# Kernel optimization log

Hardware: AMD Instinct MI355X
Metric: run time of the kernel (lower is better)

The kernel has to match this reference:

```python
import jax, jax.numpy as jnp
import numpy as np

B, C, N, V, H = 8, 256, 1024, 12, 4
D = C // H  # 64
BN_EPS = 1e-5
NEG = 1e10


def _vconv(x, W, b, g, bt, m4):
    """VointConv block: 1x1 conv + BN(batch stats) + relu, with reset_voint_mask
    applied after every sublayer (as in the torch loop).
    x: [B, Cin, N, V], W: [Cout, Cin], m4: [B, 1, N, V] float mask."""
    y = (jnp.einsum('oc,bcnv->bonv', W, x) + b[None, :, None, None]) * m4
    mu = jnp.mean(y, axis=(0, 2, 3), keepdims=True)
    var = jnp.var(y, axis=(0, 2, 3), keepdims=True)
    y = ((y - mu) * jax.lax.rsqrt(var + BN_EPS) * g[None, :, None, None]
         + bt[None, :, None, None]) * m4
    return jax.nn.relu(y) * m4


def setup_inputs() -> dict:
    key = jax.random.key(0)
    ks = jax.random.split(key, 20)
    inp = {}
    inp['voints_feats'] = jax.random.normal(ks[0], (B, C, N, V), jnp.float32)
    inp['voints_mask'] = (jax.random.uniform(ks[1], (B, N, V)) > 0.3).astype(jnp.float32)
    w = lambda k, shp: (jax.random.normal(k, shp, jnp.float32) * 0.05)
    # embed_layers[0]: VointConv([C, C/heads])
    inp['We'] = w(ks[2], (D, C)); inp['be'] = w(ks[3], (D,))
    inp['ge'] = 1.0 + 0.1 * jax.random.normal(ks[4], (D,), jnp.float32)
    inp['bne'] = 0.1 * jax.random.normal(ks[5], (D,), jnp.float32)
    # embed_atten_layers[0]: VointConv([C/heads, 3*C])
    inp['Wa'] = w(ks[6], (3 * C, D)); inp['ba'] = w(ks[7], (3 * C,))
    inp['ga'] = 1.0 + 0.1 * jax.random.normal(ks[8], (3 * C,), jnp.float32)
    inp['bna'] = 0.1 * jax.random.normal(ks[9], (3 * C,), jnp.float32)
    # to_out[0]: VointConv([C, C])
    inp['Wo'] = w(ks[10], (C, C)); inp['bo'] = w(ks[11], (C,))
    inp['go'] = 1.0 + 0.1 * jax.random.normal(ks[12], (C,), jnp.float32)
    inp['bno'] = 0.1 * jax.random.normal(ks[13], (C,), jnp.float32)
    # feedforward[0]: VointConv([C, C])
    inp['Wf'] = w(ks[14], (C, C)); inp['bf'] = w(ks[15], (C,))
    inp['gf'] = 1.0 + 0.1 * jax.random.normal(ks[16], (C,), jnp.float32)
    inp['bnf'] = 0.1 * jax.random.normal(ks[17], (C,), jnp.float32)
    return inp


def reference(voints_feats, voints_mask, We, be, ge, bne, Wa, ba, ga, bna,
              Wo, bo, go, bno, Wf, bf, gf, bnf):
    mask = voints_mask                      # [B, N, V] float
    m4 = mask[:, None, :, :]                # [B, 1, N, V]
    # embedding to per-head dim, then joint QKV projection
    emb = _vconv(voints_feats, We, be, ge, bne, m4)      # [B, D, N, V]
    qkv = _vconv(emb, Wa, ba, ga, bna, m4)               # [B, 3C, N, V]
    k, q, v = jnp.split(qkv, 3, axis=1)                  # torch.chunk order: k, q, v
    resh = lambda t: t.reshape(B, H, D, N, V)            # 'b (h d) n v -> b h d n v'
    q, k, v = resh(q), resh(k), resh(v)
    scale = float(C) ** (-0.5)
    dots = jnp.einsum('bhdnv,bhdnj->bhnvj', q, k) * scale  # [B,H,N,V,V]
    empty = jnp.sum(mask, axis=-1) == 0                  # [B, N]
    dots = jnp.where(empty[:, None, :, None, None], 0.0, dots)
    # vointsoftmax: bias broadcasts over query dim v (mask[...,None] -> [B,1,N,V,1])
    qbias = jnp.where(mask[:, None, :, :, None] > 0, 0.0, -NEG)
    attn = jax.nn.softmax(dots + qbias, axis=-1) * mask[:, None, :, :, None]
    # faithful to source: 'b h n v j, b h d n v -> b h n v d' (j summed over attn only)
    out = jnp.einsum('bhnvj,bhdnv->bhnvd', attn, v)      # [B,H,N,V,D]
    out = out.transpose(0, 1, 4, 2, 3).reshape(B, C, N, V)  # 'b h n v d -> b (h d) n v'
    out = jnp.where(empty[:, None, :, None], 0.0, out)
    out = _vconv(out, Wo, bo, go, bno, m4)
    x = voints_feats + out
    x = x + _vconv(x, Wf, bf, gf, bnf, m4)
    return x
```

## Files before the change

kernel.cpp:

```cpp
#include <hip/hip_runtime.h>
#include <hip/hip_bf16.h>

typedef __attribute__((ext_vector_type(8))) __bf16 bf16x8;
typedef __attribute__((ext_vector_type(4))) float floatx4;
typedef __attribute__((ext_vector_type(8))) unsigned short ushort8;

namespace {
constexpr int kC  = 256;
constexpr int kNV = 1024 * 12;
constexpr int kP  = 8 * kNV;
constexpr float kEps = 1e-5f;

constexpr size_t OFF_PART   = 2048;
constexpr size_t OFF_WB     = 2048 + 16384;
constexpr size_t OFF_XT     = OFF_WB + 81920;
constexpr size_t OFF_Y1     = OFF_XT + (size_t)kP * 256 / 2;
constexpr size_t OFF_Y2     = OFF_Y1 + (size_t)kP * 64 / 2;
constexpr size_t OFF_Y3     = OFF_Y2 + (size_t)kP * 256 / 2;
}

__device__ __forceinline__ unsigned short f2bf(float f) {
    unsigned int u = __builtin_bit_cast(unsigned int, f);
    u += 0x7FFFu + ((u >> 16) & 1u);
    return (unsigned short)(u >> 16);
}
__device__ __forceinline__ float bf2f(unsigned short h) {
    unsigned int u = ((unsigned int)h) << 16;
    return __builtin_bit_cast(float, u);
}

__global__ void convw_kernel(const float* __restrict__ We, const float* __restrict__ Wa,
                             const float* __restrict__ Wo, const float* __restrict__ Wf,
                             unsigned short* __restrict__ dst)
{
    const int f = (blockIdx.x * 256 + threadIdx.x) * 4;
    const float* src; int off, M, K, base;
    if (f < 16384)      { src = We;            off = f;         M = 64;  K = 256; base = 0; }
    else if (f < 32768) { src = Wa + 512 * 64; off = f - 16384; M = 256; K = 64;  base = 16384; }
    else if (f < 98304) { src = Wo;            off = f - 32768; M = 256; K = 256; base = 32768; }
    else                { src = Wf;            off = f - 98304; M = 256; K = 256; base = 98304; }
    const int m = off / K, k = off - m * K;
    const float4 v = *(const float4*)&src[off];
    ushort4 o; o.x = f2bf(v.x); o.y = f2bf(v.y); o.z = f2bf(v.z); o.w = f2bf(v.w);
    *(ushort4*)&dst[base + (k >> 5) * (M * 32) + m * 32 + (k & 31)] = o;
}

__global__ __launch_bounds__(256) void transpose_kernel(
    const float* __restrict__ x, unsigned short* __restrict__ xT)
{
    __shared__ float T[64][65];
    const int p0 = blockIdx.x * 64;
    const int c0 = blockIdx.y * 64;
    const int b  = p0 / kNV;
    const int q0 = p0 - b * kNV;
    const int t  = threadIdx.x;

    const int cl = t >> 2;
    const int pq = (t & 3) * 16;
    const float* src = &x[(size_t)(b * kC + c0 + cl) * kNV + q0 + pq];
    #pragma unroll
    for (int i = 0; i < 4; ++i) {
        const float4 v = *(const float4*)&src[i * 4];
        T[cl][pq + i * 4 + 0] = v.x;
        T[cl][pq + i * 4 + 1] = v.y;
        T[cl][pq + i * 4 + 2] = v.z;
        T[cl][pq + i * 4 + 3] = v.w;
    }
    __syncthreads();
    const int pr = t >> 2;
    const int cb = (t & 3) * 16;
    #pragma unroll
    for (int i = 0; i < 2; ++i) {
        ushort8 o;
        #pragma unroll
        for (int j = 0; j < 8; ++j) o[j] = f2bf(T[cb + i * 8 + j][pr]);
        *(ushort8*)&xT[(size_t)(p0 + pr) * 256 + c0 + cb + i * 8] = o;
    }
}

template<int MODE>
__device__ __forceinline__ ushort8 xform(ushort8 y8, ushort8 x8, float mp,
                                         const float* __restrict__ actA,
                                         const float* __restrict__ actB, int kk)
{
    if constexpr (MODE == 0) {
        return y8;
    } else {
        const float4 a0 = *(const float4*)&actA[kk];
        const float4 a1 = *(const float4*)&actA[kk + 4];
        const float4 b0 = *(const float4*)&actB[kk];
        const float4 b1 = *(const float4*)&actB[kk + 4];
        const float aa[8] = {a0.x, a0.y, a0.z, a0.w, a1.x, a1.y, a1.z, a1.w};
        const float bb[8] = {b0.x, b0.y, b0.z, b0.w, b1.x, b1.y, b1.z, b1.w};
        ushort8 o;
        #pragma unroll
        for (int j = 0; j < 8; ++j) {
            float v = bf2f(y8[j]);
            v = mp * fmaxf(fmaf(aa[j], v, bb[j]), 0.f);
            if constexpr (MODE == 2) v += bf2f(x8[j]);
            o[j] = f2bf(v);
        }
        return o;
    }
}

template<int BM, int MTOT, int K, int MODE, int SIBS, int MINW>
__global__ __launch_bounds__(256, MINW) void gemm_kernel(
    const unsigned short* __restrict__ Apk, const float* __restrict__ bias,
    const unsigned short* __restrict__ Yprev, const unsigned short* __restrict__ XT,
    const float* __restrict__ mask,
    const float* __restrict__ pPrev, const float* __restrict__ gPrev,
    const float* __restrict__ btPrev,
    unsigned short* __restrict__ Yout, float* __restrict__ partial, int slabsPerBlock)
{
    constexpr int LD = 264;
    constexpr int NT = K / 32;
    constexpr int FM = BM / 64;
    constexpr int FP = 2;
    constexpr int CH = K / 64;
    __shared__ unsigned short Bs[2][32 * LD];
    __shared__ float Sst[2][256];
    __shared__ float ActA[256];
    __shared__ float ActB[256];

    const int tid  = threadIdx.x;
    const int w    = tid >> 6, lane = tid & 63, quad = lane >> 4, lt = lane & 15;
    const int mBase = w * 16 * FM;

    Sst[0][tid] = 0.f; Sst[1][tid] = 0.f;

    int groupId, sib;
    if constexpr (SIBS > 1) {
        const int x = blockIdx.x & 7;
        const int s = blockIdx.x >> 3;
        const int perX = (int)(gridDim.x >> 3) / SIBS;
        sib = s % SIBS;
        groupId = x * perX + s / SIBS;
    } else {
        groupId = blockIdx.x; sib = 0;
    }
    const int chOff = sib * BM;
    const int slab0 = groupId * slabsPerBlock;

    if constexpr (MODE != 0) {
        if (tid < K) {
            float s = 0.f, s2 = 0.f;
            #pragma unroll
            for (int k = 0; k < 8; ++k) {
                s  += pPrev[k * 512 + tid];
                s2 += pPrev[k * 512 + 256 + tid];
            }
            const float mu  = s * (1.f / kP);
            const float var = s2 * (1.f / kP) - mu * mu;
            const float A   = rsqrtf(var + kEps) * gPrev[tid];
            ActA[tid] = A;
            ActB[tid] = fmaf(-mu, A, btPrev[tid]);
        }
        __syncthreads();
    }

    ushort8 Areg[NT][FM];
    #pragma unroll
    for (int t = 0; t < NT; ++t)
        #pragma unroll
        for (int fm = 0; fm < FM; ++fm)
            Areg[t][fm] = *(const ushort8*)&Apk[(size_t)(t * MTOT + chOff + mBase + fm * 16 + lt) * 32 + quad * 8];

    const int spb = slabsPerBlock;

    {
        const int pBase = slab0 * 32;
        #pragma unroll
        for (int i = 0; i < CH; ++i) {
            const int c = tid + i * 256;
            const int p = c / (K / 8);
            const int kq = (c % (K / 8)) * 8;
            const ushort8 y8 = *(const ushort8*)&Yprev[(size_t)(pBase + p) * K + kq];
            ushort8 o;
            if constexpr (MODE == 0) o = y8;
            else {
                ushort8 x8{};
                if constexpr (MODE == 2) x8 = *(const ushort8*)&XT[(size_t)(pBase + p) * K + kq];
                o = xform<MODE>(y8, x8, mask[pBase + p], ActA, ActB, kq);
            }
            *(ushort8*)&Bs[0][p * LD + kq] = o;
        }
    }
    __syncthreads();

    for (int s = 0; s < spb; ++s) {
        const int pBase = (slab0 + s) * 32;
        const bool hasNext = (s + 1 < spb);

        ushort8 py[CH];
        ushort8 px[(MODE == 2) ? CH : 1];
        if (hasNext) {
            const int pN = (slab0 + s + 1) * 32;
            #pragma unroll
            for (int i = 0; i < CH; ++i) {
                const int c = tid + i * 256;
                const int p = c / (K / 8);
                const int kq = (c % (K / 8)) * 8;
                py[i] = *(const ushort8*)&Yprev[(size_t)(pN + p) * K + kq];
                if constexpr (MODE == 2)
                    px[i] = *(const ushort8*)&XT[(size_t)(pN + p) * K + kq];
            }
        }

        floatx4 acc[FM][FP];
        #pragma unroll
        for (int fm = 0; fm < FM; ++fm)
            #pragma unroll
            for (int fp = 0; fp < FP; ++fp) acc[fm][fp] = (floatx4)0.f;

        const unsigned short* bs = &Bs[s & 1][0];
        #pragma unroll
        for (int t = 0; t < NT; ++t) {
            bf16x8 bF[FP];
            #pragma unroll
            for (int fp = 0; fp < FP; ++fp)
                bF[fp] = *(const bf16x8*)&bs[(fp * 16 + lt) * LD + t * 32 + quad * 8];
            #pragma unroll
            for (int fm = 0; fm < FM; ++fm) {
                const bf16x8 aF = __builtin_bit_cast(bf16x8, Areg[t][fm]);
                #pragma unroll
                for (int fp = 0; fp < FP; ++fp)
                    acc[fm][fp] = __builtin_amdgcn_mfma_f32_16x16x32_bf16(aF, bF[fp], acc[fm][fp], 0, 0, 0);
            }
        }

        float mpv[FP];
        #pragma unroll
        for (int fp = 0; fp < FP; ++fp) mpv[fp] = mask[pBase + fp * 16 + lt];

        float sS[FM][4], sQ[FM][4];
        #pragma unroll
        for (int fm = 0; fm < FM; ++fm)
            #pragma unroll
            for (int i = 0; i < 4; ++i) { sS[fm][i] = 0.f; sQ[fm][i] = 0.f; }

        #pragma unroll
        for (int fm = 0; fm < FM; ++fm) {
            const float4 bia = *(const float4*)&bias[chOff + mBase + fm * 16 + quad * 4];
            const float bi[4] = {bia.x, bia.y, bia.z, bia.w};
            #pragma unroll
            for (int fp = 0; fp < FP; ++fp) {
                const int pG = pBase + fp * 16 + lt;
                float vv[4];
                #pragma unroll
                for (int i = 0; i < 4; ++i) {
                    const float v = (acc[fm][fp][i] + bi[i]) * mpv[fp];
                    vv[i] = v; sS[fm][i] += v; sQ[fm][i] += v * v;
                }
                ushort4 o; o.x = f2bf(vv[0]); o.y = f2bf(vv[1]); o.z = f2bf(vv[2]); o.w = f2bf(vv[3]);
                *(ushort4*)&Yout[(size_t)pG * MTOT + chOff + mBase + fm * 16 + quad * 4] = o;
            }
        }
        #pragma unroll
        for (int fm = 0; fm < FM; ++fm)
            #pragma unroll
            for (int i = 0; i < 4; ++i) {
                #pragma unroll
                for (int off = 1; off < 16; off <<= 1) {
                    sS[fm][i] += __shfl_xor(sS[fm][i], off);
                    sQ[fm][i] += __shfl_xor(sQ[fm][i], off);
                }
            }
        if (lt == 0) {
            #pragma unroll
            for (int fm = 0; fm < FM; ++fm)
                #pragma unroll
                for (int i = 0; i < 4; ++i) {
                    const int ch = mBase + fm * 16 + quad * 4 + i;
                    Sst[0][ch] += sS[fm][i];
                    Sst[1][ch] += sQ[fm][i];
                }
        }

        if (hasNext) {
            const int pN = (slab0 + s + 1) * 32;
            unsigned short* bn = &Bs[(s + 1) & 1][0];
            #pragma unroll
            for (int i = 0; i < CH; ++i) {
                const int c = tid + i * 256;
                const int p = c / (K / 8);
                const int kq = (c % (K / 8)) * 8;
                ushort8 o;
                if constexpr (MODE == 0) o = py[i];
                else {
                    ushort8 x8{};
                    if constexpr (MODE == 2) x8 = px[i];
                    o = xform<MODE>(py[i], x8, mask[pN + p], ActA, ActB, kq);
                }
                *(ushort8*)&bn[p * LD + kq] = o;
            }
        }
        __syncthreads();
    }

    if (tid < BM) {
        float* pb = partial + (size_t)(blockIdx.x & 7) * 512;
        atomicAdd(&pb[chOff + tid], Sst[0][tid]);
        atomicAdd(&pb[256 + chOff + tid], Sst[1][tid]);
    }
}

__global__ __launch_bounds__(256) void final_kernel(
    const unsigned short* __restrict__ xT, const unsigned short* __restrict__ y3,
    const unsigned short* __restrict__ y4,
    const float* __restrict__ p3, const float* __restrict__ g3, const float* __restrict__ bt3,
    const float* __restrict__ p4, const float* __restrict__ g4, const float* __restrict__ bt4,
    const float* __restrict__ mask, float* __restrict__ out)
{
    constexpr int TL = 264;
    __shared__ unsigned short TX[32 * TL];
    __shared__ unsigned short T4[32 * TL];
    __shared__ float PA3[256], PB3[256], PA4[256], PB4[256];
    const int p0 = blockIdx.x * 32;
    const int b  = p0 / kNV;
    const int q0 = p0 - b * kNV;

    {
        const int m = threadIdx.x;
        float s3 = 0.f, q3 = 0.f, s4 = 0.f, q4 = 0.f;
        #pragma unroll
        for (int k = 0; k < 8; ++k) {
            s3 += p3[k * 512 + m]; q3 += p3[k * 512 + 256 + m];
            s4 += p4[k * 512 + m]; q4 += p4[k * 512 + 256 + m];
        }
        const float mu3 = s3 * (1.f / kP);
        const float A3  = rsqrtf(q3 * (1.f / kP) - mu3 * mu3 + kEps) * g3[m];
        PA3[m] = A3; PB3[m] = fmaf(-mu3, A3, bt3[m]);
        const float mu4 = s4 * (1.f / kP);
        const float A4  = rsqrtf(q4 * (1.f / kP) - mu4 * mu4 + kEps) * g4[m];
        PA4[m] = A4; PB4[m] = fmaf(-mu4, A4, bt4[m]);
    }
    __syncthreads();

    #pragma unroll
    for (int i = 0; i < 4; ++i) {
        const int idx = threadIdx.x + i * 256;
        const int p = idx >> 5, c0 = (idx & 31) * 8;
        const ushort8 x8  = *(const ushort8*)&xT[(size_t)(p0 + p) * 256 + c0];
        const ushort8 y38 = *(const ushort8*)&y3[(size_t)(p0 + p) * 256 + c0];
        const ushort8 y48 = *(const ushort8*)&y4[(size_t)(p0 + p) * 256 + c0];
        const float mp = mask[p0 + p];
        ushort8 o;
        #pragma unroll
        for (int j = 0; j < 8; ++j) {
            const int c = c0 + j;
            const float x1 = bf2f(x8[j]) + mp * fmaxf(fmaf(PA3[c], bf2f(y38[j]), PB3[c]), 0.f);
            o[j] = f2bf(x1);
        }
        *(ushort8*)&TX[p * TL + c0] = o;
        *(ushort8*)&T4[p * TL + c0] = y48;
    }
    __syncthreads();

    const int qv = (threadIdx.x & 15) * 2;
    const int cb = threadIdx.x >> 4;
    const float m0v = mask[p0 + qv], m1v = mask[p0 + qv + 1];
    #pragma unroll
    for (int j = 0; j < 16; ++j) {
        const int c = cb + j * 16;
        const float a4 = PA4[c], b4 = PB4[c];
        const size_t ro = (size_t)(b * kC + c) * kNV + q0 + qv;
        float2 o;
        o.x = bf2f(TX[qv * TL + c])       + m0v * fmaxf(fmaf(a4, bf2f(T4[qv * TL + c]), b4), 0.f);
        o.y = bf2f(TX[(qv + 1) * TL + c]) + m1v * fmaxf(fmaf(a4, bf2f(T4[(qv + 1) * TL + c]), b4), 0.f);
        *(float2*)&out[ro] = o;
    }
}

extern "C" void kernel_launch(void* const* d_in, const int* in_sizes, int n_in,
                              void* d_out, int out_size, void* d_ws, size_t ws_size,
                              hipStream_t stream)
{
    const float* x    = (const float*)d_in[0];
    const float* mask = (const float*)d_in[1];
    const float* We   = (const float*)d_in[2];
    const float* be   = (const float*)d_in[3];
    const float* ge   = (const float*)d_in[4];
    const float* bne  = (const float*)d_in[5];
    const float* Wa   = (const float*)d_in[6];
    const float* ba   = (const float*)d_in[7];
    const float* ga   = (const float*)d_in[8];
    const float* bna  = (const float*)d_in[9];
    const float* Wo   = (const float*)d_in[10];
    const float* bo   = (const float*)d_in[11];
    const float* go   = (const float*)d_in[12];
    const float* bno  = (const float*)d_in[13];
    const float* Wf   = (const float*)d_in[14];
    const float* bf   = (const float*)d_in[15];
    const float* gf   = (const float*)d_in[16];
    const float* bnf  = (const float*)d_in[17];
    float* out = (float*)d_out;
    float* ws  = (float*)d_ws;

    float* part = ws + OFF_PART;
    unsigned short* Wb = (unsigned short*)(ws + OFF_WB);
    unsigned short* xT = (unsigned short*)(ws + OFF_XT);
    unsigned short* y1 = (unsigned short*)(ws + OFF_Y1);
    unsigned short* y2 = (unsigned short*)(ws + OFF_Y2);
    unsigned short* y3 = (unsigned short*)(ws + OFF_Y3);

    hipMemsetAsync(part, 0, 16384 * sizeof(float), stream);
    convw_kernel<<<160, 256, 0, stream>>>(We, Wa, Wo, Wf, Wb);
    transpose_kernel<<<dim3(kP / 64, 4), 256, 0, stream>>>(x, xT);

    const dim3 blk(256);

    gemm_kernel<64, 64, 256, 0, 1, 4><<<1024, blk, 0, stream>>>(
        Wb, be, xT, nullptr, mask, nullptr, nullptr, nullptr, y1, part, 3);

    gemm_kernel<256, 256, 64, 1, 1, 4><<<1024, blk, 0, stream>>>(
        Wb + 16384, ba + 512, y1, nullptr, mask, part, ge, bne, y2, part + 4096, 3);

    gemm_kernel<64, 256, 256, 1, 4, 4><<<1024, blk, 0, stream>>>(
        Wb + 32768, bo, y2, nullptr, mask, part + 4096, ga + 512, bna + 512, y3, part + 8192, 12);

    gemm_kernel<64, 256, 256, 2, 4, 4><<<1024, blk, 0, stream>>>(
        Wb + 98304, bf, y3, xT, mask, part + 8192, go, bno, y2, part + 12288, 12);

    final_kernel<<<kP / 32, blk, 0, stream>>>(
        xT, y3, y2, part + 8192, go, bno, part + 12288, gf, bnf, mask, out);
}
```

Before: 400.1 us.

## Retile GEMMs to 128-channel blocks, defer stat reduction, use packed bf16 convert

Changes the GEMM tiling to 128-channel blocks with two sibling blocks per slab group and adjusts the grid and slab counts, trading fewer redundant B-tile loads against occupancy. The per-slab shuffle reduction and shared-memory stat accumulation are replaced by register accumulation across all slabs, with one shuffle reduction and atomics at the end. Bias is hoisted into registers, and scalar bf16 rounding is replaced by the packed v_cvt_pk_bf16_f32 instruction. Larger FM raises register pressure, and launch bounds drop to 3 waves for the K=256 kernels.

New measurement: 389.2 us. -2.7%, faster.

```diff
diff --git a/kernel.cpp b/kernel.cpp
--- a/kernel.cpp
+++ b/kernel.cpp
@@ -27,6 +27,11 @@
 __device__ __forceinline__ float bf2f(unsigned short h) {
     unsigned int u = ((unsigned int)h) << 16;
     return __builtin_bit_cast(float, u);
+}
+__device__ __forceinline__ unsigned int f2bf2(float lo, float hi) {
+    unsigned int r;
+    asm("v_cvt_pk_bf16_f32 %0, %1, %2" : "=v"(r) : "v"(lo), "v"(hi));
+    return r;
 }
 
 __global__ void convw_kernel(const float* __restrict__ We, const float* __restrict__ Wa,
@@ -92,15 +97,17 @@
         const float4 b1 = *(const float4*)&actB[kk + 4];
         const float aa[8] = {a0.x, a0.y, a0.z, a0.w, a1.x, a1.y, a1.z, a1.w};
         const float bb[8] = {b0.x, b0.y, b0.z, b0.w, b1.x, b1.y, b1.z, b1.w};
-        ushort8 o;
+        float v[8];
         #pragma unroll
         for (int j = 0; j < 8; ++j) {
-            float v = bf2f(y8[j]);
-            v = mp * fmaxf(fmaf(aa[j], v, bb[j]), 0.f);
-            if constexpr (MODE == 2) v += bf2f(x8[j]);
-            o[j] = f2bf(v);
-        }
-        return o;
+            float t = mp * fmaxf(fmaf(aa[j], bf2f(y8[j]), bb[j]), 0.f);
+            if constexpr (MODE == 2) t += bf2f(x8[j]);
+            v[j] = t;
+        }
+        uint4 u;
+        u.x = f2bf2(v[0], v[1]); u.y = f2bf2(v[2], v[3]);
+        u.z = f2bf2(v[4], v[5]); u.w = f2bf2(v[6], v[7]);
+        return __builtin_bit_cast(ushort8, u);
     }
 }
 
@@ -119,15 +126,12 @@
     constexpr int FP = 2;
     constexpr int CH = K / 64;
     __shared__ unsigned short Bs[2][32 * LD];
-    __shared__ float Sst[2][256];
     __shared__ float ActA[256];
     __shared__ float ActB[256];
 
     const int tid  = threadIdx.x;
     const int w    = tid >> 6, lane = tid & 63, quad = lane >> 4, lt = lane & 15;
     const int mBase = w * 16 * FM;
-
-    Sst[0][tid] = 0.f; Sst[1][tid] = 0.f;
 
     int groupId, sib;
     if constexpr (SIBS > 1) {
@@ -165,6 +169,19 @@
         #pragma unroll
         for (int fm = 0; fm < FM; ++fm)
             Areg[t][fm] = *(const ushort8*)&Apk[(size_t)(t * MTOT + chOff + mBase + fm * 16 + lt) * 32 + quad * 8];
+
+    float biR[FM][4];
+    #pragma unroll
+    for (int fm = 0; fm < FM; ++fm) {
+        const float4 b4 = *(const float4*)&bias[chOff + mBase + fm * 16 + quad * 4];
+        biR[fm][0] = b4.x; biR[fm][1] = b4.y; biR[fm][2] = b4.z; biR[fm][3] = b4.w;
+    }
+
+    float aS[FM][4], aQ[FM][4];
+    #pragma unroll
+    for (int fm = 0; fm < FM; ++fm)
+        #pragma unroll
+        for (int i = 0; i < 4; ++i) { aS[fm][i] = 0.f; aQ[fm][i] = 0.f; }
 
     const int spb = slabsPerBlock;
 
@@ -233,48 +250,20 @@
         #pragma unroll
         for (int fp = 0; fp < FP; ++fp) mpv[fp] = mask[pBase + fp * 16 + lt];
 
-        float sS[FM][4], sQ[FM][4];
-        #pragma unroll
-        for (int fm = 0; fm < FM; ++fm)
-            #pragma unroll
-            for (int i = 0; i < 4; ++i) { sS[fm][i] = 0.f; sQ[fm][i] = 0.f; }
-
         #pragma unroll
         for (int fm = 0; fm < FM; ++fm) {
-            const float4 bia = *(const float4*)&bias[chOff + mBase + fm * 16 + quad * 4];
-            const float bi[4] = {bia.x, bia.y, bia.z, bia.w};
             #pragma unroll
             for (int fp = 0; fp < FP; ++fp) {
                 const int pG = pBase + fp * 16 + lt;
                 float vv[4];
                 #pragma unroll
                 for (int i = 0; i < 4; ++i) {
-                    const float v = (acc[fm][fp][i] + bi[i]) * mpv[fp];
-                    vv[i] = v; sS[fm][i] += v; sQ[fm][i] += v * v;
+                    const float v = (acc[fm][fp][i] + biR[fm][i]) * mpv[fp];
+                    vv[i] = v; aS[fm][i] += v; aQ[fm][i] += v * v;
                 }
-                ushort4 o; o.x = f2bf(vv[0]); o.y = f2bf(vv[1]); o.z = f2bf(vv[2]); o.w = f2bf(vv[3]);
-                *(ushort4*)&Yout[(size_t)pG * MTOT + chOff + mBase + fm * 16 + quad * 4] = o;
-            }
-        }
-        #pragma unroll
-        for (int fm = 0; fm < FM; ++fm)
-            #pragma unroll
-            for (int i = 0; i < 4; ++i) {
-                #pragma unroll
-                for (int off = 1; off < 16; off <<= 1) {
-                    sS[fm][i] += __shfl_xor(sS[fm][i], off);
-                    sQ[fm][i] += __shfl_xor(sQ[fm][i], off);
-                }
-            }
-        if (lt == 0) {
-            #pragma unroll
-            for (int fm = 0; fm < FM; ++fm)
-                #pragma unroll
-                for (int i = 0; i < 4; ++i) {
-                    const int ch = mBase + fm * 16 + quad * 4 + i;
-                    Sst[0][ch] += sS[fm][i];
-                    Sst[1][ch] += sQ[fm][i];
-                }
+                uint2 o; o.x = f2bf2(vv[0], vv[1]); o.y = f2bf2(vv[2], vv[3]);
+                *(uint2*)&Yout[(size_t)pG * MTOT + chOff + mBase + fm * 16 + quad * 4] = o;
+            }
         }
 
         if (hasNext) {
@@ -298,10 +287,26 @@
         __syncthreads();
     }
 
-    if (tid < BM) {
+    #pragma unroll
+    for (int fm = 0; fm < FM; ++fm)
+        #pragma unroll
+        for (int i = 0; i < 4; ++i) {
+            #pragma unroll
+            for (int off = 1; off < 16; off <<= 1) {
+                aS[fm][i] += __shfl_xor(aS[fm][i], off);
+                aQ[fm][i] += __shfl_xor(aQ[fm][i], off);
+            }
+        }
+    if (lt == 0) {
         float* pb = partial + (size_t)(blockIdx.x & 7) * 512;
-        atomicAdd(&pb[chOff + tid], Sst[0][tid]);
-        atomicAdd(&pb[256 + chOff + tid], Sst[1][tid]);
+        #pragma unroll
+        for (int fm = 0; fm < FM; ++fm)
+            #pragma unroll
+            for (int i = 0; i < 4; ++i) {
+                const int ch = chOff + mBase + fm * 16 + quad * 4 + i;
+                atomicAdd(&pb[ch], aS[fm][i]);
+                atomicAdd(&pb[256 + ch], aQ[fm][i]);
+            }
     }
 }
 
@@ -413,14 +418,14 @@
     gemm_kernel<64, 64, 256, 0, 1, 4><<<1024, blk, 0, stream>>>(
         Wb, be, xT, nullptr, mask, nullptr, nullptr, nullptr, y1, part, 3);
 
-    gemm_kernel<256, 256, 64, 1, 1, 4><<<1024, blk, 0, stream>>>(
-        Wb + 16384, ba + 512, y1, nullptr, mask, part, ge, bne, y2, part + 4096, 3);
-
-    gemm_kernel<64, 256, 256, 1, 4, 4><<<1024, blk, 0, stream>>>(
-        Wb + 32768, bo, y2, nullptr, mask, part + 4096, ga + 512, bna + 512, y3, part + 8192, 12);
-
-    gemm_kernel<64, 256, 256, 2, 4, 4><<<1024, blk, 0, stream>>>(
-        Wb + 98304, bf, y3, xT, mask, part + 8192, go, bno, y2, part + 12288, 12);
+    gemm_kernel<128, 256, 64, 1, 2, 4><<<1024, blk, 0, stream>>>(
+        Wb + 16384, ba + 512, y1, nullptr, mask, part, ge, bne, y2, part + 4096, 6);
+
+    gemm_kernel<128, 256, 256, 1, 2, 3><<<768, blk, 0, stream>>>(
+        Wb + 32768, bo, y2, nullptr, mask, part + 4096, ga + 512, bna + 512, y3, part + 8192, 8);
+
+    gemm_kernel<128, 256, 256, 2, 2, 3><<<768, blk, 0, stream>>>(
+        Wb + 98304, bf, y3, xT, mask, part + 8192, go, bno, y2, part + 12288, 8);
 
     final_kernel<<<kP / 32, blk, 0, stream>>>(
         xT, y3, y2, part + 8192, go, bno, part + 12288, gf, bnf, mask, out);
```
